# Performance work log

Hardware: AMD Instinct MI355X
Metric: run time of the kernel (lower is better)

Reference implementation:

```python
import jax, jax.numpy as jnp
import numpy as np

L = 16384      # sequence length
CH = 512       # input channels
S = 128        # SSM state dim


def setup_inputs() -> dict:
    key = jax.random.key(0)
    kx, kb, kc, kdt = jax.random.split(key, 4)
    x = jax.random.normal(kx, (L, CH), dtype=jnp.float32)
    # logA init matches flax param init: log(1 + arange(state_dim))
    logA = jnp.log(1.0 + jnp.arange(S, dtype=jnp.float32))
    # Dense (no bias) kernels, lecun-normal-ish scale 1/sqrt(fan_in)
    scale = 1.0 / np.sqrt(CH)
    WB = jax.random.normal(kb, (CH, S), dtype=jnp.float32) * scale
    WC = jax.random.normal(kc, (CH, S), dtype=jnp.float32) * scale
    Wdt = jax.random.normal(kdt, (CH, 1), dtype=jnp.float32) * scale
    bdt = jnp.zeros((1,), dtype=jnp.float32)
    return {"x": x, "logA": logA, "WB": WB, "WC": WC, "Wdt": Wdt, "bdt": bdt}


def reference(x, logA, WB, WC, Wdt, bdt):
    A = -jnp.exp(logA)                      # (S,)
    B = x @ WB                              # (L, S)
    C = x @ WC                              # (L, S)
    dt = jax.nn.softplus(x @ Wdt + bdt)     # (L, 1), learned since dt=None
    Abar = jnp.exp(A * dt)                  # (L, S) discretized transition
    Bbar = (Abar - 1.0) * B / A             # (L, S) discretized input term

    def scan_fn(el1, el2):
        (A1, B1), (A2, B2) = el1, el2
        return (A1 * A2, A1 * B2)           # faithful to source (non-standard combine)

    _, AkB = jax.lax.associative_scan(scan_fn, (Abar, Bbar))  # over axis 0 (L)
    return jnp.einsum('ls,ls,lc->lc', C, AkB, x)              # (L, CH)
```

## Files before the change

kernel.cpp:

```cpp
#include <hip/hip_runtime.h>
#include <math.h>

#define L_SEQ  16384
#define CHN    512
#define S_DIM  128
#define NPRE   1024
#define FBLK   2048
#define E_CUT  104.0f

static __device__ __forceinline__ float softplus_f(float z) {
    return (z > 20.f) ? z : log1pf(expf(z));
}

__global__ __launch_bounds__(256) void k_fill_dt(const float* __restrict__ x,
                                                 const float* __restrict__ Wdt,
                                                 const float* __restrict__ bdt,
                                                 float* __restrict__ dt,
                                                 float* __restrict__ out)
{
    const int b = blockIdx.x;
    const int t = threadIdx.x;

    {
        float4* o4 = (float4*)out;
        const float4 z = make_float4(0.f, 0.f, 0.f, 0.f);
        size_t i = (size_t)b * 256 + t;
#pragma unroll
        for (int k = 0; k < 4; ++k) {
            o4[i] = z;
            i += (size_t)FBLK * 256;
        }
    }

    if (b < NPRE / 4) {
        const int wave = t >> 6, lane = t & 63;
        const int row  = b * 4 + wave;
        const float4* xr = (const float4*)(x + (size_t)row * CHN);
        const float4* w4 = (const float4*)Wdt;
        float acc = 0.f;
#pragma unroll
        for (int i = 0; i < 2; ++i) {
            float4 xv = xr[lane + 64 * i];
            float4 wv = w4[lane + 64 * i];
            acc = fmaf(xv.x, wv.x, acc); acc = fmaf(xv.y, wv.y, acc);
            acc = fmaf(xv.z, wv.z, acc); acc = fmaf(xv.w, wv.w, acc);
        }
#pragma unroll
        for (int off = 32; off; off >>= 1) acc += __shfl_down(acc, off);
        if (lane == 0) dt[row] = softplus_f(acc + bdt[0]);
    }
}

__global__ __launch_bounds__(64) void k_scan_fb(const float* __restrict__ x,
                                                const float* __restrict__ Wdt,
                                                const float* __restrict__ bdt,
                                                float* __restrict__ dt,
                                                float* __restrict__ E,
                                                int*   __restrict__ n_p)
{
    const int lane = threadIdx.x;
    const int PER  = NPRE / 64;

    float v[PER], ex[PER];
    const float4* dt4 = (const float4*)dt;
#pragma unroll
    for (int i = 0; i < PER / 4; ++i) {
        float4 q = dt4[lane * (PER / 4) + i];
        v[4*i+0] = q.x; v[4*i+1] = q.y; v[4*i+2] = q.z; v[4*i+3] = q.w;
    }

    float run = 0.f;
#pragma unroll
    for (int i = 0; i < PER; ++i) { ex[i] = run; run += v[i]; }

    float incl = run;
#pragma unroll
    for (int off = 1; off < 64; off <<= 1) {
        float o = __shfl_up(incl, off);
        if (lane >= off) incl += o;
    }
    const float excl  = incl - run;
    const float total = __shfl(incl, 63);

    float4* E4 = (float4*)E;
#pragma unroll
    for (int i = 0; i < PER / 4; ++i)
        E4[lane * (PER / 4) + i] = make_float4(excl + ex[4*i],   excl + ex[4*i+1],
                                               excl + ex[4*i+2], excl + ex[4*i+3]);

    int cnt = 0;
#pragma unroll
    for (int i = 0; i < PER; ++i) cnt += (excl + ex[i] < E_CUT) ? 1 : 0;
#pragma unroll
    for (int off = 32; off; off >>= 1) cnt += __shfl_down(cnt, off);
    int n = __shfl(cnt, 0);

    if (n == NPRE) {
        float running = total;
        for (int l = NPRE; l < L_SEQ && running < E_CUT; ++l) {
            const float4* xr = (const float4*)(x + (size_t)l * CHN);
            const float4* w4 = (const float4*)Wdt;
            float acc = 0.f;
#pragma unroll
            for (int i = 0; i < 2; ++i) {
                float4 xv = xr[lane + 64 * i];
                float4 wv = w4[lane + 64 * i];
                acc = fmaf(xv.x, wv.x, acc); acc = fmaf(xv.y, wv.y, acc);
                acc = fmaf(xv.z, wv.z, acc); acc = fmaf(xv.w, wv.w, acc);
            }
#pragma unroll
            for (int off = 32; off; off >>= 1) acc += __shfl_down(acc, off);
            float d = softplus_f(__shfl(acc, 0) + bdt[0]);
            if (lane == 0) { E[l] = running; dt[l] = d; }
            running += d;
            ++n;
        }
    }
    if (lane == 0) n_p[0] = n;
}

__global__ __launch_bounds__(256) void k_active(const float* __restrict__ x,
                                                const float* __restrict__ logA,
                                                const float* __restrict__ WB,
                                                const float* __restrict__ WC,
                                                const float* __restrict__ dt,
                                                const float* __restrict__ E,
                                                const int* __restrict__ n_p,
                                                float* __restrict__ out)
{
    const int n  = n_p[0];
    const int t  = threadIdx.x;
    const int g  = t >> 5;
    const int s4 = t & 31;

    __shared__ float  xs[CHN];
    __shared__ float4 redB[8][32];
    __shared__ float4 redC[8][32];
    __shared__ float  scal;

    const float4* wb = (const float4*)WB;
    const float4* wc = (const float4*)WC;

    for (int l = blockIdx.x; l < n; l += gridDim.x) {
        ((float2*)xs)[t] = ((const float2*)(x + (size_t)l * CHN))[t];
        __syncthreads();

        float4 aB = make_float4(0.f, 0.f, 0.f, 0.f);
        float4 aC = make_float4(0.f, 0.f, 0.f, 0.f);
#pragma unroll 8
        for (int c = g; c < CHN; c += 8) {
            const float  xc = xs[c];
            const float4 bq = wb[c * 32 + s4];
            const float4 cq = wc[c * 32 + s4];
            aB.x = fmaf(xc, bq.x, aB.x);  aB.y = fmaf(xc, bq.y, aB.y);
            aB.z = fmaf(xc, bq.z, aB.z);  aB.w = fmaf(xc, bq.w, aB.w);
            aC.x = fmaf(xc, cq.x, aC.x);  aC.y = fmaf(xc, cq.y, aC.y);
            aC.z = fmaf(xc, cq.z, aC.z);  aC.w = fmaf(xc, cq.w, aC.w);
        }
        redB[g][s4] = aB;
        redC[g][s4] = aC;
        __syncthreads();

        if (t < 32) {
            float4 B = redB[0][t], C = redC[0][t];
#pragma unroll
            for (int k = 1; k < 8; ++k) {
                float4 bq = redB[k][t], cq = redC[k][t];
                B.x += bq.x; B.y += bq.y; B.z += bq.z; B.w += bq.w;
                C.x += cq.x; C.y += cq.y; C.z += cq.z; C.w += cq.w;
            }
            const float  e   = E[l];
            const float  dtl = dt[l];
            const float4 la  = ((const float4*)logA)[t];

            float con = 0.f;
            float a = -expf(la.x);
            con = fmaf(C.x * expf(a * e), expm1f(a * dtl) * B.x / a, con);
            a = -expf(la.y);
            con = fmaf(C.y * expf(a * e), expm1f(a * dtl) * B.y / a, con);
            a = -expf(la.z);
            con = fmaf(C.z * expf(a * e), expm1f(a * dtl) * B.z / a, con);
            a = -expf(la.w);
            con = fmaf(C.w * expf(a * e), expm1f(a * dtl) * B.w / a, con);
#pragma unroll
            for (int off = 16; off; off >>= 1) con += __shfl_down(con, off);
            if (t == 0) scal = con;
        }
        __syncthreads();

        const float  sc = scal;
        const float2 xv = ((float2*)xs)[t];
        ((float2*)(out + (size_t)l * CHN))[t] = make_float2(sc * xv.x, sc * xv.y);
        __syncthreads();
    }
}

extern "C" void kernel_launch(void* const* d_in, const int* in_sizes, int n_in,
                              void* d_out, int out_size, void* d_ws, size_t ws_size,
                              hipStream_t stream)
{
    const float* x    = (const float*)d_in[0];
    const float* logA = (const float*)d_in[1];
    const float* WB   = (const float*)d_in[2];
    const float* WC   = (const float*)d_in[3];
    const float* Wdt  = (const float*)d_in[4];
    const float* bdt  = (const float*)d_in[5];
    float* out = (float*)d_out;

    float* dt  = (float*)d_ws;
    float* E   = dt + L_SEQ;
    int*   n_p = (int*)(E + L_SEQ);

    k_fill_dt<<<FBLK, 256, 0, stream>>>(x, Wdt, bdt, dt, out);
    k_scan_fb<<<1,    64,  0, stream>>>(x, Wdt, bdt, dt, E, n_p);
    k_active <<<256,  256, 0, stream>>>(x, logA, WB, WC, dt, E, n_p, out);
}
```

Baseline: 34.50 us.

## Fuse dt prefix scan into active kernel with per-block redundant scan

Removes the single-block scan kernel and folds the prefix sum of the first 1024 dt values into the active-row kernel. Every block now redundantly computes the scan in shared memory using a wave scan plus a cross-wave offset, and counts active rows with a shared atomic. Active-row E and dt values are read from shared memory instead of global memory. This drops one kernel launch and the serial one-wave dependency between kernels. The cost is redundant scan work in every block, and the rare fallback path runs its sequential loop in all blocks, each writing the same values to global memory.

New measurement: 32.35 us (median of 2 runs). -6.2%, faster.

```diff
diff --git a/kernel.cpp b/kernel.cpp
--- a/kernel.cpp
+++ b/kernel.cpp
@@ -6,6 +6,7 @@
 #define S_DIM  128
 #define NPRE   1024
 #define FBLK   2048
+#define ABLK   256
 #define E_CUT  104.0f
 
 static __device__ __forceinline__ float softplus_f(float z) {
@@ -51,92 +52,91 @@
     }
 }
 
-__global__ __launch_bounds__(64) void k_scan_fb(const float* __restrict__ x,
-                                                const float* __restrict__ Wdt,
-                                                const float* __restrict__ bdt,
-                                                float* __restrict__ dt,
-                                                float* __restrict__ E,
-                                                int*   __restrict__ n_p)
+__global__ __launch_bounds__(256) void k_scan_active(const float* __restrict__ x,
+                                                     const float* __restrict__ logA,
+                                                     const float* __restrict__ WB,
+                                                     const float* __restrict__ WC,
+                                                     const float* __restrict__ Wdt,
+                                                     const float* __restrict__ bdt,
+                                                     float* __restrict__ dtg,
+                                                     float* __restrict__ Eg,
+                                                     float* __restrict__ out)
 {
-    const int lane = threadIdx.x;
-    const int PER  = NPRE / 64;
-
-    float v[PER], ex[PER];
-    const float4* dt4 = (const float4*)dt;
-#pragma unroll
-    for (int i = 0; i < PER / 4; ++i) {
-        float4 q = dt4[lane * (PER / 4) + i];
-        v[4*i+0] = q.x; v[4*i+1] = q.y; v[4*i+2] = q.z; v[4*i+3] = q.w;
-    }
-
-    float run = 0.f;
-#pragma unroll
-    for (int i = 0; i < PER; ++i) { ex[i] = run; run += v[i]; }
-
-    float incl = run;
-#pragma unroll
-    for (int off = 1; off < 64; off <<= 1) {
-        float o = __shfl_up(incl, off);
-        if (lane >= off) incl += o;
-    }
-    const float excl  = incl - run;
-    const float total = __shfl(incl, 63);
-
-    float4* E4 = (float4*)E;
-#pragma unroll
-    for (int i = 0; i < PER / 4; ++i)
-        E4[lane * (PER / 4) + i] = make_float4(excl + ex[4*i],   excl + ex[4*i+1],
-                                               excl + ex[4*i+2], excl + ex[4*i+3]);
-
-    int cnt = 0;
-#pragma unroll
-    for (int i = 0; i < PER; ++i) cnt += (excl + ex[i] < E_CUT) ? 1 : 0;
-#pragma unroll
-    for (int off = 32; off; off >>= 1) cnt += __shfl_down(cnt, off);
-    int n = __shfl(cnt, 0);
-
-    if (n == NPRE) {
-        float running = total;
-        for (int l = NPRE; l < L_SEQ && running < E_CUT; ++l) {
-            const float4* xr = (const float4*)(x + (size_t)l * CHN);
-            const float4* w4 = (const float4*)Wdt;
-            float acc = 0.f;
-#pragma unroll
-            for (int i = 0; i < 2; ++i) {
-                float4 xv = xr[lane + 64 * i];
-                float4 wv = w4[lane + 64 * i];
-                acc = fmaf(xv.x, wv.x, acc); acc = fmaf(xv.y, wv.y, acc);
-                acc = fmaf(xv.z, wv.z, acc); acc = fmaf(xv.w, wv.w, acc);
-            }
-#pragma unroll
-            for (int off = 32; off; off >>= 1) acc += __shfl_down(acc, off);
-            float d = softplus_f(__shfl(acc, 0) + bdt[0]);
-            if (lane == 0) { E[l] = running; dt[l] = d; }
-            running += d;
-            ++n;
-        }
-    }
-    if (lane == 0) n_p[0] = n;
-}
-
-__global__ __launch_bounds__(256) void k_active(const float* __restrict__ x,
-                                                const float* __restrict__ logA,
-                                                const float* __restrict__ WB,
-                                                const float* __restrict__ WC,
-                                                const float* __restrict__ dt,
-                                                const float* __restrict__ E,
-                                                const int* __restrict__ n_p,
-                                                float* __restrict__ out)
-{
-    const int n  = n_p[0];
-    const int t  = threadIdx.x;
-    const int g  = t >> 5;
-    const int s4 = t & 31;
-
+    const int t    = threadIdx.x;
+    const int lane = t & 63;
+    const int wid  = t >> 6;
+
+    __shared__ float  dt_s[NPRE];
+    __shared__ float  E_s[NPRE];
+    __shared__ float  wsum[4];
+    __shared__ int    n_s;
     __shared__ float  xs[CHN];
     __shared__ float4 redB[8][32];
     __shared__ float4 redC[8][32];
     __shared__ float  scal;
+
+    if (t == 0) n_s = 0;
+    const float4 q = ((const float4*)dtg)[t];
+    const float tsum = q.x + q.y + q.z + q.w;
+
+    float incl = tsum;
+#pragma unroll
+    for (int off = 1; off < 64; off <<= 1) {
+        float o = __shfl_up(incl, off);
+        if (lane >= off) incl += o;
+    }
+    if (lane == 63) wsum[wid] = incl;
+    __syncthreads();
+
+    float woff = 0.f;
+    for (int w = 0; w < wid; ++w) woff += wsum[w];
+    const float excl = woff + incl - tsum;
+
+    dt_s[4*t+0] = q.x;  dt_s[4*t+1] = q.y;  dt_s[4*t+2] = q.z;  dt_s[4*t+3] = q.w;
+    E_s[4*t+0] = excl;
+    E_s[4*t+1] = excl + q.x;
+    E_s[4*t+2] = excl + q.x + q.y;
+    E_s[4*t+3] = excl + q.x + q.y + q.z;
+
+    int cnt = (E_s[4*t+0] < E_CUT) + (E_s[4*t+1] < E_CUT)
+            + (E_s[4*t+2] < E_CUT) + (E_s[4*t+3] < E_CUT);
+#pragma unroll
+    for (int off = 32; off; off >>= 1) cnt += __shfl_down(cnt, off);
+    if (lane == 0) atomicAdd(&n_s, cnt);
+    __syncthreads();
+    int n = n_s;
+
+    if (n == NPRE) {
+        if (wid == 0) {
+            float running = E_s[NPRE - 1] + dt_s[NPRE - 1];
+            int nn = NPRE;
+            for (int l = NPRE; l < L_SEQ && running < E_CUT; ++l) {
+                const float4* xr = (const float4*)(x + (size_t)l * CHN);
+                const float4* w4 = (const float4*)Wdt;
+                float acc = 0.f;
+#pragma unroll
+                for (int i = 0; i < 2; ++i) {
+                    float4 xv = xr[lane + 64 * i];
+                    float4 wv = w4[lane + 64 * i];
+                    acc = fmaf(xv.x, wv.x, acc); acc = fmaf(xv.y, wv.y, acc);
+                    acc = fmaf(xv.z, wv.z, acc); acc = fmaf(xv.w, wv.w, acc);
+                }
+#pragma unroll
+                for (int off = 32; off; off >>= 1) acc += __shfl_down(acc, off);
+                float d = softplus_f(__shfl(acc, 0) + bdt[0]);
+                if (lane == 0) { Eg[l] = running; dtg[l] = d; }
+                running += d;
+                ++nn;
+            }
+            if (lane == 0) n_s = nn;
+        }
+        __threadfence_block();
+        __syncthreads();
+        n = n_s;
+    }
+
+    const int g  = t >> 5;
+    const int s4 = t & 31;
 
     const float4* wb = (const float4*)WB;
     const float4* wc = (const float4*)WC;
@@ -169,8 +169,8 @@
                 B.x += bq.x; B.y += bq.y; B.z += bq.z; B.w += bq.w;
                 C.x += cq.x; C.y += cq.y; C.z += cq.z; C.w += cq.w;
             }
-            const float  e   = E[l];
-            const float  dtl = dt[l];
+            const float  e   = (l < NPRE) ? E_s[l]  : Eg[l];
+            const float  dtl = (l < NPRE) ? dt_s[l] : dtg[l];
             const float4 la  = ((const float4*)logA)[t];
 
             float con = 0.f;
@@ -207,11 +207,10 @@
     const float* bdt  = (const float*)d_in[5];
     float* out = (float*)d_out;
 
-    float* dt  = (float*)d_ws;
-    float* E   = dt + L_SEQ;
-    int*   n_p = (int*)(E + L_SEQ);
-
-    k_fill_dt<<<FBLK, 256, 0, stream>>>(x, Wdt, bdt, dt, out);
-    k_scan_fb<<<1,    64,  0, stream>>>(x, Wdt, bdt, dt, E, n_p);
-    k_active <<<256,  256, 0, stream>>>(x, logA, WB, WC, dt, E, n_p, out);
-}
+    float* dt = (float*)d_ws;
+    float* E  = dt + L_SEQ;
+
+    k_fill_dt    <<<FBLK, 256, 0, stream>>>(x, Wdt, bdt, dt, out);
+    k_scan_active<<<ABLK, 256, 0, stream>>>(x, logA, WB, WC, Wdt, bdt,
+                                            dt, E, out);
+}
```
